# Kernel tuning notes

Measured on AMD Instinct MI355X. Metric: run time of the kernel, lower is better.

The kernel has to match this reference:

```python
import jax, jax.numpy as jnp
import numpy as np

NUM_EMBED = 1024
EMBED_DIM = 256
DECAY = 0.99
EPS = 1e-05
COMMIT = 0.25


def setup_inputs() -> dict:
    key = jax.random.key(0)
    k1, k2, k3 = jax.random.split(key, 3)
    z = jax.random.normal(k1, (64, 32, 32, EMBED_DIM), dtype=jnp.float32)
    lim = 1.0 / NUM_EMBED
    embeddings = jax.random.uniform(k2, (NUM_EMBED, EMBED_DIM), minval=-lim, maxval=lim, dtype=jnp.float32)
    ema_embed = jax.random.uniform(k3, (NUM_EMBED, EMBED_DIM), minval=-lim, maxval=lim, dtype=jnp.float32)
    cluster_size = jnp.zeros((NUM_EMBED,), dtype=jnp.float32)
    return {"z": z, "embeddings": embeddings, "ema_embed": ema_embed, "cluster_size": cluster_size}


def reference(z, embeddings, ema_embed, cluster_size):
    B, H, W, D = z.shape
    zf = z.reshape(-1, D)  # [N, D]
    # squared euclidean distances to codebook: [N, K]
    distances = (zf ** 2).sum(-1, keepdims=True) + (embeddings ** 2).sum(-1) - 2.0 * (zf @ embeddings.T)
    closest = jnp.argmin(distances, axis=-1)  # [N] int
    quantized_indices = closest.reshape(B, H, W)[:, None]  # [B,1,H,W]
    quantized = embeddings[closest].reshape(z.shape)  # gather instead of one-hot GEMM

    # --- training-mode EMA codebook update (buffer math, no grads) ---
    n_i = jnp.zeros((NUM_EMBED,), dtype=zf.dtype).at[closest].add(1.0)  # per-code counts
    new_cluster = cluster_size * DECAY + n_i * (1.0 - DECAY)
    dw = jnp.zeros_like(embeddings).at[closest].add(zf)  # scatter-add of assigned vectors
    new_ema = ema_embed * DECAY + dw * (1.0 - DECAY)
    n = new_cluster.sum()
    new_cluster = (new_cluster + EPS) / (n + NUM_EMBED * EPS) * n
    new_embeddings = new_ema / new_cluster[:, None]

    commitment_loss = jnp.mean((quantized - z) ** 2)
    st_quantized = z + jax.lax.stop_gradient(quantized - z)  # straight-through
    loss = commitment_loss * COMMIT
    return loss, st_quantized, quantized_indices, new_embeddings, new_cluster, new_ema
```

## Files before the change

kernel.cpp:

```cpp
#include <hip/hip_runtime.h>
#include <float.h>
#include <stdint.h>

#define K_EMB 1024
#define D_EMB 256

typedef _Float16 half8 __attribute__((ext_vector_type(8)));
typedef float f32x4_t __attribute__((ext_vector_type(4)));

typedef const __attribute__((address_space(1))) void* as1cv;
typedef __attribute__((address_space(3))) void* as3v;


__global__ void convert_e_kernel(const float* __restrict__ e, _Float16* __restrict__ ehp,
                                 float* __restrict__ t2, unsigned int* __restrict__ flag_cnt) {
  if (blockIdx.x == 0 && threadIdx.x == 0) { flag_cnt[0] = 0; flag_cnt[1] = 0; }
  int row = blockIdx.x * 4 + (threadIdx.x >> 6);
  int lane = threadIdx.x & 63;
  float4 v = ((const float4*)(e + (size_t)row * D_EMB))[lane];
  float s = v.x * v.x + v.y * v.y + v.z * v.z + v.w * v.w;
#pragma unroll
  for (int off = 32; off > 0; off >>= 1) s += __shfl_down(s, off, 64);
  if (lane == 0) t2[row] = s;
  _Float16* dst = ehp + (size_t)row * D_EMB + lane * 4;
  dst[0] = (_Float16)v.x; dst[1] = (_Float16)v.y;
  dst[2] = (_Float16)v.z; dst[3] = (_Float16)v.w;
}


#define BM 64
#define CCH 16
#define NCH (K_EMB / CCH)
#define DELTA 1.5e-4f
#define ADELTA 7.6e-5f

__launch_bounds__(128, 3)
__global__ void argmin_mfma_kernel(const float* __restrict__ z,
                                   const _Float16* __restrict__ eh,
                                   int* __restrict__ closest,
                                   float* __restrict__ idx_out,
                                   unsigned int* __restrict__ flag_cnt,
                                   unsigned int* __restrict__ flag_row,
                                   unsigned int* __restrict__ flag_cand,
                                   unsigned int* __restrict__ flag2) {
  __shared__ _Float16 ebuf[3][CCH * D_EMB];
  const int tid = threadIdx.x;
  const int wid = tid >> 6;
  const int lane = tid & 63;
  const int c = lane & 15, g = lane >> 4;
  const int row0 = blockIdx.x * BM + wid * 32;

  half8 A[2][8];
#pragma unroll
  for (int fr = 0; fr < 2; ++fr)
#pragma unroll
    for (int df = 0; df < 8; ++df) {
      const float* zp = z + (size_t)(row0 + fr * 16 + c) * D_EMB + df * 32 + g * 8;
      const float4 v0 = *(const float4*)zp;
      const float4 v1 = *(const float4*)(zp + 4);
      half8 h;
      h[0] = (_Float16)v0.x; h[1] = (_Float16)v0.y; h[2] = (_Float16)v0.z; h[3] = (_Float16)v0.w;
      h[4] = (_Float16)v1.x; h[5] = (_Float16)v1.y; h[6] = (_Float16)v1.z; h[7] = (_Float16)v1.w;
      A[fr][df] = h;
    }

  float m1[8], m2[8], m3[8];
  int k1[8], k2[8];
#pragma unroll
  for (int s = 0; s < 8; ++s) { m1[s] = -FLT_MAX; m2[s] = -FLT_MAX; m3[s] = -FLT_MAX; k1[s] = 0; k2[s] = 0; }

#define INS(s, dvv, kkv)                                        \
  {                                                             \
    const float dv_ = (dvv); const int kk_ = (kkv);             \
    const bool gt1 = dv_ > m1[s];                               \
    const bool gt2 = dv_ > m2[s];                               \
    m3[s] = __builtin_amdgcn_fmed3f(m2[s], m3[s], dv_);         \
    const float nm2 = __builtin_amdgcn_fmed3f(m1[s], m2[s], dv_); \
    k2[s] = gt1 ? k1[s] : (gt2 ? kk_ : k2[s]);                  \
    m2[s] = nm2;                                                \
    m1[s] = fmaxf(m1[s], dv_);                                  \
    k1[s] = gt1 ? kk_ : k1[s];                                  \
  }

  const int rswz = (c & 7) << 3;

  int sgs[4];
#pragma unroll
  for (int u = 0; u < 4; ++u) {
    const int gidx = (wid * 4 + u) * 64 + lane;
    sgs[u] = (gidx & ~7) | ((gidx & 7) ^ ((gidx >> 5) & 7));
  }

#define ISSUE(cbn, buf)                                                              \
  {                                                                                  \
    const _Float16* src_ = eh + (size_t)(cbn) * (CCH * D_EMB);                       \
    _Float16* db_ = &ebuf[buf][0];                                                   \
    _Pragma("unroll")                                                                \
    for (int u = 0; u < 4; ++u)                                                      \
      __builtin_amdgcn_global_load_lds((as1cv)(src_ + (size_t)sgs[u] * 8),           \
                                       (as3v)(db_ + (wid * 4 + u) * 512), 16, 0, 0); \
  }

#define COMPUTE(rb_, cb_)                                                            \
  {                                                                                  \
    f32x4_t a0 = (f32x4_t){0.f, 0.f, 0.f, 0.f};                                      \
    f32x4_t a1 = (f32x4_t){0.f, 0.f, 0.f, 0.f};                                      \
    _Pragma("unroll")                                                                \
    for (int d = 0; d < 8; ++d) {                                                    \
      const int elem = (d * 32 + g * 8) ^ rswz;                                      \
      const half8 Bh = *(const half8*)(&ebuf[rb_][c * D_EMB + elem]);                \
      a0 = __builtin_amdgcn_mfma_f32_16x16x32_f16(A[0][d], Bh, a0, 0, 0, 0);         \
      a1 = __builtin_amdgcn_mfma_f32_16x16x32_f16(A[1][d], Bh, a1, 0, 0, 0);         \
    }                                                                                \
    const int kk = (cb_)*CCH + c;                                                    \
    _Pragma("unroll")                                                                \
    for (int r = 0; r < 4; ++r) {                                                    \
      INS(r, a0[r], kk)                                                              \
      INS(4 + r, a1[r], kk)                                                          \
    }                                                                                \
  }

  ISSUE(0, 0)
  ISSUE(1, 1)

  for (int cb = 0; cb < NCH - 1; ++cb) {
    asm volatile("s_waitcnt vmcnt(4)" ::: "memory");
    __builtin_amdgcn_s_barrier();
    __builtin_amdgcn_sched_barrier(0);
    if (cb + 2 < NCH) ISSUE(cb + 2, (cb + 2) % 3)
    const int rb = cb % 3;
    COMPUTE(rb, cb)
  }
  asm volatile("s_waitcnt vmcnt(0)" ::: "memory");
  __builtin_amdgcn_s_barrier();
  __builtin_amdgcn_sched_barrier(0);
  {
    const int rb = (NCH - 1) % 3;
    COMPUTE(rb, NCH - 1)
  }
#undef COMPUTE
#undef ISSUE

#pragma unroll
  for (int m = 1; m <= 8; m <<= 1) {
#pragma unroll
    for (int s = 0; s < 8; ++s) {
      const float om1 = __shfl_xor(m1[s], m, 64);
      const int ok1 = __shfl_xor(k1[s], m, 64);
      const float om2 = __shfl_xor(m2[s], m, 64);
      const int ok2 = __shfl_xor(k2[s], m, 64);
      const float om3 = __shfl_xor(m3[s], m, 64);
      INS(s, om1, ok1)
      INS(s, om2, ok2)
      m3[s] = fmaxf(m3[s], om3);
    }
  }
#undef INS

  if (c == 0) {
#pragma unroll
    for (int s = 0; s < 8; ++s) {
      const int fr = s >> 2, r = s & 3;
      const int row = row0 + fr * 16 + g * 4 + r;
      closest[row] = k1[s];
      idx_out[row] = (float)k1[s];
      if (m1[s] - m2[s] < ADELTA) {
        if (m1[s] - m3[s] < ADELTA) {
          const unsigned int p = atomicAdd(&flag_cnt[1], 1u);
          flag2[p] = (unsigned int)row;
        } else {
          const unsigned int p = atomicAdd(&flag_cnt[0], 1u);
          flag_row[p] = (unsigned int)row;
          flag_cand[p] = (unsigned int)k1[s] | ((unsigned int)k2[s] << 10);
        }
      }
    }
  }
}


__launch_bounds__(256, 4)
__global__ void fixup_kernel(const float* __restrict__ z, const float* __restrict__ emb,
                             const float* __restrict__ t2,
                             const unsigned int* __restrict__ flag_cnt,
                             const unsigned int* __restrict__ flag1_row,
                             const unsigned int* __restrict__ flag1_cand,
                             const unsigned int* __restrict__ flag2,
                             int* __restrict__ closest, float* __restrict__ idx_out) {
  const int tid = threadIdx.x;
  {
    const int q = tid & 3;
    const unsigned int cnt = flag_cnt[0];
    const unsigned int nquads = (gridDim.x * 256) >> 2;
    for (unsigned int i = (blockIdx.x * 256 + tid) >> 2; i < cnt; i += nquads) {
      const int row = (int)flag1_row[i];
      const unsigned int cand = flag1_cand[i];
      const int ka = (int)(cand & 1023u), kb = (int)((cand >> 10) & 1023u);
      const float4* zp = (const float4*)(z + (size_t)row * D_EMB) + q * 16;
      const float4* ap = (const float4*)(emb + (size_t)ka * D_EMB) + q * 16;
      const float4* bp = (const float4*)(emb + (size_t)kb * D_EMB) + q * 16;
      float s0 = 0.f, sa = 0.f, sb = 0.f;
#pragma unroll 8
      for (int u = 0; u < 16; ++u) {
        const float4 zv = zp[u], av = ap[u], bv = bp[u];
        s0 = fmaf(zv.x, zv.x, s0); s0 = fmaf(zv.y, zv.y, s0);
        s0 = fmaf(zv.z, zv.z, s0); s0 = fmaf(zv.w, zv.w, s0);
        sa = fmaf(zv.x, av.x, sa); sa = fmaf(zv.y, av.y, sa);
        sa = fmaf(zv.z, av.z, sa); sa = fmaf(zv.w, av.w, sa);
        sb = fmaf(zv.x, bv.x, sb); sb = fmaf(zv.y, bv.y, sb);
        sb = fmaf(zv.z, bv.z, sb); sb = fmaf(zv.w, bv.w, sb);
      }
#pragma unroll
      for (int m = 1; m <= 2; m <<= 1) {
        s0 += __shfl_xor(s0, m, 64);
        sa += __shfl_xor(sa, m, 64);
        sb += __shfl_xor(sb, m, 64);
      }
      if (q == 0) {
        const float da = (s0 + t2[ka]) - 2.f * sa;
        const float db = (s0 + t2[kb]) - 2.f * sb;
        int kbest = ka;
        if (db < da || (db == da && kb < ka)) kbest = kb;
        closest[row] = kbest;
        idx_out[row] = (float)kbest;
      }
    }
  }
  __shared__ float zs[D_EMB];
  __shared__ float t1s;
  __shared__ float redm[4];
  __shared__ int redk[4];
  const int lane = tid & 63, wv = tid >> 6;
  const unsigned int cnt2 = flag_cnt[1];
  for (unsigned int j = blockIdx.x; j < cnt2; j += gridDim.x) {
    __syncthreads();
    const int row = (int)flag2[j];
    if (wv == 0) {
      const float4 v = ((const float4*)(z + (size_t)row * D_EMB))[lane];
      ((float4*)zs)[lane] = v;
      float s = v.x * v.x + v.y * v.y + v.z * v.z + v.w * v.w;
#pragma unroll
      for (int off = 32; off > 0; off >>= 1) s += __shfl_down(s, off, 64);
      if (lane == 0) t1s = s;
    }
    __syncthreads();
    const float4* e0 = (const float4*)(emb + (size_t)(4 * tid + 0) * D_EMB);
    const float4* e1 = (const float4*)(emb + (size_t)(4 * tid + 1) * D_EMB);
    const float4* e2 = (const float4*)(emb + (size_t)(4 * tid + 2) * D_EMB);
    const float4* e3 = (const float4*)(emb + (size_t)(4 * tid + 3) * D_EMB);
    const float4* zp4 = (const float4*)zs;
    float a0 = 0.f, a1 = 0.f, a2 = 0.f, a3 = 0.f;
    for (int i = 0; i < 64; ++i) {
      const float4 z4 = zp4[i];
      const float4 v0 = e0[i], v1 = e1[i], v2 = e2[i], v3 = e3[i];
      a0 = fmaf(z4.x, v0.x, a0); a0 = fmaf(z4.y, v0.y, a0);
      a0 = fmaf(z4.z, v0.z, a0); a0 = fmaf(z4.w, v0.w, a0);
      a1 = fmaf(z4.x, v1.x, a1); a1 = fmaf(z4.y, v1.y, a1);
      a1 = fmaf(z4.z, v1.z, a1); a1 = fmaf(z4.w, v1.w, a1);
      a2 = fmaf(z4.x, v2.x, a2); a2 = fmaf(z4.y, v2.y, a2);
      a2 = fmaf(z4.z, v2.z, a2); a2 = fmaf(z4.w, v2.w, a2);
      a3 = fmaf(z4.x, v3.x, a3); a3 = fmaf(z4.y, v3.y, a3);
      a3 = fmaf(z4.z, v3.z, a3); a3 = fmaf(z4.w, v3.w, a3);
    }
    const float t1v = t1s;
    float best = FLT_MAX;
    int bk = 0x7fffffff;
    const float dvs[4] = {(t1v + t2[4 * tid + 0]) - 2.f * a0,
                          (t1v + t2[4 * tid + 1]) - 2.f * a1,
                          (t1v + t2[4 * tid + 2]) - 2.f * a2,
                          (t1v + t2[4 * tid + 3]) - 2.f * a3};
#pragma unroll
    for (int cc = 0; cc < 4; ++cc) {
      const int k = 4 * tid + cc;
      if (dvs[cc] < best) { best = dvs[cc]; bk = k; }
    }
#pragma unroll
    for (int m = 1; m <= 32; m <<= 1) {
      const float ob = __shfl_xor(best, m, 64);
      const int ok = __shfl_xor(bk, m, 64);
      if (ob < best || (ob == best && ok < bk)) { best = ob; bk = ok; }
    }
    if (lane == 0) { redm[wv] = best; redk[wv] = bk; }
    __syncthreads();
    if (tid == 0) {
      float b = redm[0];
      int k = redk[0];
#pragma unroll
      for (int w = 1; w < 4; ++w)
        if (redm[w] < b || (redm[w] == b && redk[w] < k)) { b = redm[w]; k = redk[w]; }
      closest[row] = k;
      idx_out[row] = (float)k;
    }
  }
}


__global__ void hist1_kernel(const int* __restrict__ closest, unsigned int* __restrict__ rank,
                             unsigned int* __restrict__ blockhist) {
  __shared__ unsigned int lh[K_EMB];
  const int t = threadIdx.x;
  lh[t] = 0;
  __syncthreads();
  const int row = blockIdx.x * 1024 + t;
  rank[row] = atomicAdd(&lh[closest[row]], 1u);
  __syncthreads();
  blockhist[blockIdx.x * K_EMB + t] = lh[t];
}

__global__ void hist2_kernel(unsigned int* __restrict__ blockhist, const float* __restrict__ cs,
                             unsigned int* __restrict__ base, float* __restrict__ newc,
                             float* __restrict__ o_ncl, int nblocks) {
  __shared__ unsigned int sc[K_EMB];
  __shared__ float fr[K_EMB];
  const int bin = threadIdx.x;
  unsigned int s = 0;
  if (nblocks == 64) {
    unsigned int v[64];
#pragma unroll
    for (int b = 0; b < 64; ++b) v[b] = blockhist[b * K_EMB + bin];
#pragma unroll
    for (int b = 0; b < 64; ++b) { const unsigned int t = v[b]; blockhist[b * K_EMB + bin] = s; s += t; }
  } else {
    for (int b = 0; b < nblocks; ++b) {
      const unsigned int v = blockhist[b * K_EMB + bin];
      blockhist[b * K_EMB + bin] = s;
      s += v;
    }
  }
  sc[bin] = s;
  __syncthreads();
  for (int off = 1; off < K_EMB; off <<= 1) {
    const unsigned int t = (bin >= off) ? sc[bin - off] : 0u;
    __syncthreads();
    sc[bin] += t;
    __syncthreads();
  }
  base[bin] = sc[bin] - s;
  const float pre = cs[bin] * 0.99f + (float)s * (float)(1.0 - 0.99);
  fr[bin] = pre;
  __syncthreads();
  for (int st = 512; st > 0; st >>= 1) {
    if (bin < st) fr[bin] += fr[bin + st];
    __syncthreads();
  }
  const float n = fr[0];
  const float ncl = (pre + 1e-5f) / (n + (float)(K_EMB * 1e-5)) * n;
  newc[bin] = ncl;
  o_ncl[bin] = ncl;
}

__global__ void hist3_kernel(const int* __restrict__ closest, const unsigned int* __restrict__ rank,
                             const unsigned int* __restrict__ blockhist,
                             const unsigned int* __restrict__ base,
                             unsigned int* __restrict__ sorted) {
  const int t = threadIdx.x;
  const int row = blockIdx.x * 1024 + t;
  const int k = closest[row];
  sorted[base[k] + blockhist[blockIdx.x * K_EMB + k] + rank[row]] = (unsigned int)row;
}


__global__ void dwsum_kernel(const float* __restrict__ z, const unsigned int* __restrict__ sorted,
                             const unsigned int* __restrict__ base, const float* __restrict__ ema,
                             const float* __restrict__ newc, const float* __restrict__ emb,
                             float* __restrict__ o_st, float* __restrict__ o_nema,
                             float* __restrict__ o_nemb, float* __restrict__ loss_part, int N) {
  const int k = blockIdx.x;
  const int lane = threadIdx.x & 63, wv = threadIdx.x >> 6;
  const unsigned int b0 = base[k];
  const unsigned int b1 = (k == K_EMB - 1) ? (unsigned int)N : base[k + 1];
  const float4 ev = ((const float4*)(emb + (size_t)k * D_EMB))[lane];
  float4 acc = {0.f, 0.f, 0.f, 0.f};
  float ls = 0.f;
  for (unsigned int j = b0 + wv; j < b1; j += 4) {
    const unsigned int row = sorted[j];
    const float4 zv = ((const float4*)(z + (size_t)row * D_EMB))[lane];
    const float dx = ev.x - zv.x, dy = ev.y - zv.y, dz = ev.z - zv.z, dww = ev.w - zv.w;
    float* sp = o_st + (size_t)row * D_EMB + lane * 4;
    sp[0] = zv.x + dx; sp[1] = zv.y + dy; sp[2] = zv.z + dz; sp[3] = zv.w + dww;
    ls = fmaf(dx, dx, ls); ls = fmaf(dy, dy, ls);
    ls = fmaf(dz, dz, ls); ls = fmaf(dww, dww, ls);
    acc.x += zv.x; acc.y += zv.y; acc.z += zv.z; acc.w += zv.w;
  }
  __shared__ float4 red[256];
  __shared__ float lred[256];
  red[threadIdx.x] = acc;
  lred[threadIdx.x] = ls;
  __syncthreads();
  for (int s = 128; s > 0; s >>= 1) {
    if (threadIdx.x < s) lred[threadIdx.x] += lred[threadIdx.x + s];
    __syncthreads();
  }
  if (threadIdx.x == 0) loss_part[k] = lred[0];
  if (wv == 0) {
    const float4 a1 = red[64 + lane], a2 = red[128 + lane], a3 = red[192 + lane];
    acc = red[lane];
    acc.x += a1.x + a2.x + a3.x;
    acc.y += a1.y + a2.y + a3.y;
    acc.z += a1.z + a2.z + a3.z;
    acc.w += a1.w + a2.w + a3.w;
    const float4 emv = ((const float4*)ema)[k * 64 + lane];
    const float nc = newc[k];
    const int off = k * D_EMB + lane * 4;
    float ne;
    ne = emv.x * 0.99f + acc.x * (float)(1.0 - 0.99); o_nema[off + 0] = ne; o_nemb[off + 0] = ne / nc;
    ne = emv.y * 0.99f + acc.y * (float)(1.0 - 0.99); o_nema[off + 1] = ne; o_nemb[off + 1] = ne / nc;
    ne = emv.z * 0.99f + acc.z * (float)(1.0 - 0.99); o_nema[off + 2] = ne; o_nemb[off + 2] = ne / nc;
    ne = emv.w * 0.99f + acc.w * (float)(1.0 - 0.99); o_nema[off + 3] = ne; o_nemb[off + 3] = ne / nc;
  }
}

__global__ void loss_final_kernel(const float* __restrict__ loss_part,
                                  float* __restrict__ o_loss, int nrows) {
  const int i = threadIdx.x;
  __shared__ double dred[1024];
  dred[i] = (double)loss_part[i];
  __syncthreads();
  for (int s = 512; s > 0; s >>= 1) {
    if (i < s) dred[i] += dred[i + s];
    __syncthreads();
  }
  if (i == 0) o_loss[0] = (float)(0.25 * (dred[0] / ((double)nrows * (double)D_EMB)));
}


extern "C" void kernel_launch(void* const* d_in, const int* in_sizes, int n_in,
                              void* d_out, int out_size, void* d_ws, size_t ws_size,
                              hipStream_t stream) {
  const float* z = (const float*)d_in[0];
  const float* emb = (const float*)d_in[1];
  const float* ema = (const float*)d_in[2];
  const float* cs = (const float*)d_in[3];
  const int N = in_sizes[0] / D_EMB;
  const int NB = N / 1024;

  float* out = (float*)d_out;
  float* o_loss = out;
  float* o_st = out + 1;
  float* o_idx = o_st + (size_t)N * D_EMB;
  float* o_nemb = o_idx + N;
  float* o_ncl = o_nemb + (size_t)K_EMB * D_EMB;
  float* o_nema = o_ncl + K_EMB;

  float* ws = (float*)d_ws;
  float* t2 = ws;
  float* newc = t2 + K_EMB;
  float* loss_part = newc + K_EMB;
  unsigned int* flag_cnt = (unsigned int*)(loss_part + K_EMB);
  unsigned int* basep = flag_cnt + 4;
  _Float16* ehp = (_Float16*)(basep + K_EMB);
  int* closest = (int*)(ehp + (size_t)K_EMB * D_EMB);
  unsigned int* flag_row = (unsigned int*)(closest + N);
  unsigned int* flag_cand = flag_row + N;
  unsigned int* sorted = flag_cand + N;
  unsigned int* flag2 = sorted + N;

  unsigned int* rank = flag_row;
  unsigned int* blockhist = flag_cand;

  convert_e_kernel<<<K_EMB / 4, 256, 0, stream>>>(emb, ehp, t2, flag_cnt);
  argmin_mfma_kernel<<<N / BM, 128, 0, stream>>>(z, ehp, closest, o_idx,
                                                 flag_cnt, flag_row, flag_cand, flag2);
  fixup_kernel<<<256, 256, 0, stream>>>(z, emb, t2, flag_cnt, flag_row, flag_cand, flag2,
                                        closest, o_idx);
  hist1_kernel<<<NB, 1024, 0, stream>>>(closest, rank, blockhist);
  hist2_kernel<<<1, 1024, 0, stream>>>(blockhist, cs, basep, newc, o_ncl, NB);
  hist3_kernel<<<NB, 1024, 0, stream>>>(closest, rank, blockhist, basep, sorted);
  dwsum_kernel<<<K_EMB, 256, 0, stream>>>(z, sorted, basep, ema, newc, emb,
                                          o_st, o_nema, o_nemb, loss_part, N);
  loss_final_kernel<<<1, 1024, 0, stream>>>(loss_part, o_loss, N);
}
```

Baseline: 183.8 us.

## Use single-wave argmin blocks without barriers and widen dwsum to 512 threads

The argmin kernel now runs one 64-lane wave per block covering 32 rows. That wave loads each 16-code chunk into a double-buffered LDS area on its own, so no workgroup barriers are needed. It reads the B fragments into registers before refilling the same buffer. This removes barrier stalls between waves, but each row tile now moves twice as much codebook data from global memory into LDS. Separately, dwsum uses 512 threads with 8 waves striding the sorted rows and prefetches the next row index to shorten the dependent load chain.

```diff
diff --git a/kernel.cpp b/kernel.cpp
--- a/kernel.cpp
+++ b/kernel.cpp
@@ -28,13 +28,12 @@
 }
 
 
-#define BM 64
 #define CCH 16
 #define NCH (K_EMB / CCH)
 #define DELTA 1.5e-4f
 #define ADELTA 7.6e-5f
 
-__launch_bounds__(128, 3)
+__launch_bounds__(64, 3)
 __global__ void argmin_mfma_kernel(const float* __restrict__ z,
                                    const _Float16* __restrict__ eh,
                                    int* __restrict__ closest,
@@ -43,12 +42,10 @@
                                    unsigned int* __restrict__ flag_row,
                                    unsigned int* __restrict__ flag_cand,
                                    unsigned int* __restrict__ flag2) {
-  __shared__ _Float16 ebuf[3][CCH * D_EMB];
-  const int tid = threadIdx.x;
-  const int wid = tid >> 6;
-  const int lane = tid & 63;
+  __shared__ _Float16 ebuf[2][CCH * D_EMB];
+  const int lane = threadIdx.x;
   const int c = lane & 15, g = lane >> 4;
-  const int row0 = blockIdx.x * BM + wid * 32;
+  const int row0 = blockIdx.x * 32;
 
   half8 A[2][8];
 #pragma unroll
@@ -84,10 +81,10 @@
 
   const int rswz = (c & 7) << 3;
 
-  int sgs[4];
-#pragma unroll
-  for (int u = 0; u < 4; ++u) {
-    const int gidx = (wid * 4 + u) * 64 + lane;
+  int sgs[8];
+#pragma unroll
+  for (int u = 0; u < 8; ++u) {
+    const int gidx = u * 64 + lane;
     sgs[u] = (gidx & ~7) | ((gidx & 7) ^ ((gidx >> 5) & 7));
   }
 
@@ -96,49 +93,62 @@
     const _Float16* src_ = eh + (size_t)(cbn) * (CCH * D_EMB);                       \
     _Float16* db_ = &ebuf[buf][0];                                                   \
     _Pragma("unroll")                                                                \
-    for (int u = 0; u < 4; ++u)                                                      \
+    for (int u = 0; u < 8; ++u)                                                      \
       __builtin_amdgcn_global_load_lds((as1cv)(src_ + (size_t)sgs[u] * 8),           \
-                                       (as3v)(db_ + (wid * 4 + u) * 512), 16, 0, 0); \
-  }
-
-#define COMPUTE(rb_, cb_)                                                            \
-  {                                                                                  \
-    f32x4_t a0 = (f32x4_t){0.f, 0.f, 0.f, 0.f};                                      \
-    f32x4_t a1 = (f32x4_t){0.f, 0.f, 0.f, 0.f};                                      \
-    _Pragma("unroll")                                                                \
-    for (int d = 0; d < 8; ++d) {                                                    \
-      const int elem = (d * 32 + g * 8) ^ rswz;                                      \
-      const half8 Bh = *(const half8*)(&ebuf[rb_][c * D_EMB + elem]);                \
-      a0 = __builtin_amdgcn_mfma_f32_16x16x32_f16(A[0][d], Bh, a0, 0, 0, 0);         \
-      a1 = __builtin_amdgcn_mfma_f32_16x16x32_f16(A[1][d], Bh, a1, 0, 0, 0);         \
-    }                                                                                \
-    const int kk = (cb_)*CCH + c;                                                    \
-    _Pragma("unroll")                                                                \
-    for (int r = 0; r < 4; ++r) {                                                    \
-      INS(r, a0[r], kk)                                                              \
-      INS(4 + r, a1[r], kk)                                                          \
-    }                                                                                \
+                                       (as3v)(db_ + u * 512), 16, 0, 0);             \
   }
 
   ISSUE(0, 0)
   ISSUE(1, 1)
 
   for (int cb = 0; cb < NCH - 1; ++cb) {
-    asm volatile("s_waitcnt vmcnt(4)" ::: "memory");
-    __builtin_amdgcn_s_barrier();
+    asm volatile("s_waitcnt vmcnt(8)" ::: "memory");
+    half8 Bh[8];
+#pragma unroll
+    for (int d = 0; d < 8; ++d) {
+      const int elem = (d * 32 + g * 8) ^ rswz;
+      Bh[d] = *(const half8*)(&ebuf[cb & 1][c * D_EMB + elem]);
+    }
+    asm volatile("s_waitcnt lgkmcnt(0)" ::: "memory");
     __builtin_amdgcn_sched_barrier(0);
-    if (cb + 2 < NCH) ISSUE(cb + 2, (cb + 2) % 3)
-    const int rb = cb % 3;
-    COMPUTE(rb, cb)
-  }
-  asm volatile("s_waitcnt vmcnt(0)" ::: "memory");
-  __builtin_amdgcn_s_barrier();
-  __builtin_amdgcn_sched_barrier(0);
+    if (cb + 2 < NCH) ISSUE(cb + 2, cb & 1)
+    f32x4_t a0 = (f32x4_t){0.f, 0.f, 0.f, 0.f};
+    f32x4_t a1 = (f32x4_t){0.f, 0.f, 0.f, 0.f};
+#pragma unroll
+    for (int d = 0; d < 8; ++d) {
+      a0 = __builtin_amdgcn_mfma_f32_16x16x32_f16(A[0][d], Bh[d], a0, 0, 0, 0);
+      a1 = __builtin_amdgcn_mfma_f32_16x16x32_f16(A[1][d], Bh[d], a1, 0, 0, 0);
+    }
+    const int kk = cb * CCH + c;
+#pragma unroll
+    for (int r = 0; r < 4; ++r) {
+      INS(r, a0[r], kk)
+      INS(4 + r, a1[r], kk)
+    }
+  }
   {
-    const int rb = (NCH - 1) % 3;
-    COMPUTE(rb, NCH - 1)
-  }
-#undef COMPUTE
+    asm volatile("s_waitcnt vmcnt(0)" ::: "memory");
+    const int cb = NCH - 1;
+    half8 Bh[8];
+#pragma unroll
+    for (int d = 0; d < 8; ++d) {
+      const int elem = (d * 32 + g * 8) ^ rswz;
+      Bh[d] = *(const half8*)(&ebuf[cb & 1][c * D_EMB + elem]);
+    }
+    f32x4_t a0 = (f32x4_t){0.f, 0.f, 0.f, 0.f};
+    f32x4_t a1 = (f32x4_t){0.f, 0.f, 0.f, 0.f};
+#pragma unroll
+    for (int d = 0; d < 8; ++d) {
+      a0 = __builtin_amdgcn_mfma_f32_16x16x32_f16(A[0][d], Bh[d], a0, 0, 0, 0);
+      a1 = __builtin_amdgcn_mfma_f32_16x16x32_f16(A[1][d], Bh[d], a1, 0, 0, 0);
+    }
+    const int kk = cb * CCH + c;
+#pragma unroll
+    for (int r = 0; r < 4; ++r) {
+      INS(r, a0[r], kk)
+      INS(4 + r, a1[r], kk)
+    }
+  }
 #undef ISSUE
 
 #pragma unroll
@@ -360,6 +370,7 @@
 }
 
 
+__launch_bounds__(512)
 __global__ void dwsum_kernel(const float* __restrict__ z, const unsigned int* __restrict__ sorted,
                              const unsigned int* __restrict__ base, const float* __restrict__ ema,
                              const float* __restrict__ newc, const float* __restrict__ emb,
@@ -372,8 +383,12 @@
   const float4 ev = ((const float4*)(emb + (size_t)k * D_EMB))[lane];
   float4 acc = {0.f, 0.f, 0.f, 0.f};
   float ls = 0.f;
-  for (unsigned int j = b0 + wv; j < b1; j += 4) {
-    const unsigned int row = sorted[j];
+  unsigned int j = b0 + wv;
+  unsigned int nextrow = (j < b1) ? sorted[j] : 0u;
+  while (j < b1) {
+    const unsigned int row = nextrow;
+    const unsigned int jn = j + 8;
+    if (jn < b1) nextrow = sorted[jn];
     const float4 zv = ((const float4*)(z + (size_t)row * D_EMB))[lane];
     const float dx = ev.x - zv.x, dy = ev.y - zv.y, dz = ev.z - zv.z, dww = ev.w - zv.w;
     float* sp = o_st + (size_t)row * D_EMB + lane * 4;
@@ -381,24 +396,25 @@
     ls = fmaf(dx, dx, ls); ls = fmaf(dy, dy, ls);
     ls = fmaf(dz, dz, ls); ls = fmaf(dww, dww, ls);
     acc.x += zv.x; acc.y += zv.y; acc.z += zv.z; acc.w += zv.w;
-  }
-  __shared__ float4 red[256];
-  __shared__ float lred[256];
+    j = jn;
+  }
+  __shared__ float4 red[512];
+  __shared__ float lred[512];
   red[threadIdx.x] = acc;
   lred[threadIdx.x] = ls;
   __syncthreads();
-  for (int s = 128; s > 0; s >>= 1) {
+  for (int s = 256; s > 0; s >>= 1) {
     if (threadIdx.x < s) lred[threadIdx.x] += lred[threadIdx.x + s];
     __syncthreads();
   }
   if (threadIdx.x == 0) loss_part[k] = lred[0];
   if (wv == 0) {
-    const float4 a1 = red[64 + lane], a2 = red[128 + lane], a3 = red[192 + lane];
     acc = red[lane];
-    acc.x += a1.x + a2.x + a3.x;
-    acc.y += a1.y + a2.y + a3.y;
-    acc.z += a1.z + a2.z + a3.z;
-    acc.w += a1.w + a2.w + a3.w;
+#pragma unroll
+    for (int w = 1; w < 8; ++w) {
+      const float4 aw = red[w * 64 + lane];
+      acc.x += aw.x; acc.y += aw.y; acc.z += aw.z; acc.w += aw.w;
+    }
     const float4 emv = ((const float4*)ema)[k * 64 + lane];
     const float nc = newc[k];
     const int off = k * D_EMB + lane * 4;
@@ -459,14 +475,14 @@
   unsigned int* blockhist = flag_cand;
 
   convert_e_kernel<<<K_EMB / 4, 256, 0, stream>>>(emb, ehp, t2, flag_cnt);
-  argmin_mfma_kernel<<<N / BM, 128, 0, stream>>>(z, ehp, closest, o_idx,
-                                                 flag_cnt, flag_row, flag_cand, flag2);
+  argmin_mfma_kernel<<<N / 32, 64, 0, stream>>>(z, ehp, closest, o_idx,
+                                                flag_cnt, flag_row, flag_cand, flag2);
   fixup_kernel<<<256, 256, 0, stream>>>(z, emb, t2, flag_cnt, flag_row, flag_cand, flag2,
                                         closest, o_idx);
   hist1_kernel<<<NB, 1024, 0, stream>>>(closest, rank, blockhist);
   hist2_kernel<<<1, 1024, 0, stream>>>(blockhist, cs, basep, newc, o_ncl, NB);
   hist3_kernel<<<NB, 1024, 0, stream>>>(closest, rank, blockhist, basep, sorted);
-  dwsum_kernel<<<K_EMB, 256, 0, stream>>>(z, sorted, basep, ema, newc, emb,
+  dwsum_kernel<<<K_EMB, 512, 0, stream>>>(z, sorted, basep, ema, newc, emb,
                                           o_st, o_nema, o_nemb, loss_part, N);
   loss_final_kernel<<<1, 1024, 0, stream>>>(loss_part, o_loss, N);
 }
```

Result: slower. 198.9 us (+8.2%).
